# Kernel tuning notes

Hardware: AMD Instinct MI355X
Metric: run time of the kernel (lower is better)

The kernel has to match this reference:

```python
import jax, jax.numpy as jnp
import numpy as np

D = 1024      # embedding_dim
H = 16        # num_heads
DH = D // H   # head_dim
DFF = 4 * D
EPS = 1e-5


def setup_inputs() -> dict:
    key = jax.random.key(0)
    ks = jax.random.split(key, 10)
    B, T = 2, 2048
    s = 0.02
    return {
        "x": jax.random.normal(ks[0], (B, T, D), dtype=jnp.float32),
        "Wq": jax.random.normal(ks[1], (H, D, DH), dtype=jnp.float32) * s,
        "Wk": jax.random.normal(ks[2], (H, D, DH), dtype=jnp.float32) * s,
        "Wv": jax.random.normal(ks[3], (H, D, DH), dtype=jnp.float32) * s,
        "W1": jax.random.normal(ks[4], (D, DFF), dtype=jnp.float32) * s,
        "b1": jnp.zeros((DFF,), dtype=jnp.float32),
        "W2": jax.random.normal(ks[5], (DFF, D), dtype=jnp.float32) * s,
        "b2": jnp.zeros((D,), dtype=jnp.float32),
        "gamma1": jnp.ones((D,), dtype=jnp.float32),
        "beta1": jnp.zeros((D,), dtype=jnp.float32),
        "gamma2": jnp.ones((D,), dtype=jnp.float32),
        "beta2": jnp.zeros((D,), dtype=jnp.float32),
    }


def _layernorm(x, gamma, beta):
    # torch.var default is unbiased (ddof=1) -- faithful to LayerNorm1d
    mean = jnp.mean(x, axis=-1, keepdims=True)
    var = jnp.var(x, axis=-1, keepdims=True, ddof=1)
    return gamma * (x - mean) * jax.lax.rsqrt(var + EPS) + beta


def _block(x, Wq, Wk, Wv, W1, b1, W2, b2, gamma1, beta1, gamma2, beta2):
    B, T, _ = x.shape
    h = _layernorm(x, gamma1, beta1)
    # per-head projections stacked: [B,H,T,DH]
    Q = jnp.einsum('btd,hde->bhte', h, Wq)
    K = jnp.einsum('btd,hde->bhte', h, Wk)
    V = jnp.einsum('btd,hde->bhte', h, Wv)
    # NOTE: original scales by 1/sqrt(embedding_dim), NOT head_dim
    scores = jnp.einsum('bhqe,bhke->bhqk', Q, K) / jnp.sqrt(jnp.float32(D))
    causal = jnp.tril(jnp.ones((T, T), dtype=bool))
    scores = jnp.where(causal, scores, -jnp.inf)
    attn = jax.nn.softmax(scores, axis=-1)
    out = jnp.einsum('bhqk,bhke->bhqe', attn, V)
    # torch.cat over heads along last dim == transpose+reshape
    out = out.transpose(0, 2, 1, 3).reshape(B, T, D)
    x = x + out
    h2 = _layernorm(x, gamma2, beta2)
    ff = jax.nn.relu(h2 @ W1 + b1) @ W2 + b2  # dropout is identity at inference
    return x + ff


def reference(x, Wq, Wk, Wv, W1, b1, W2, b2, gamma1, beta1, gamma2, beta2):
    return _block(x, Wq, Wk, Wv, W1, b1, W2, b2, gamma1, beta1, gamma2, beta2)
```

## Files before the change

kernel.cpp:

```cpp
#include <hip/hip_runtime.h>

typedef unsigned short u16;
typedef __bf16 bf16;
typedef __attribute__((ext_vector_type(8))) __bf16 bf16x8;
typedef __attribute__((ext_vector_type(4))) float f32x4;
typedef __attribute__((ext_vector_type(8))) unsigned short u16x8;
typedef unsigned long long u64;

__device__ __forceinline__ float bf2f(u16 h) {
  return __uint_as_float(((unsigned int)h) << 16);
}
__device__ __forceinline__ u16 f2bf(float f) {
  unsigned int u = __float_as_uint(f);
  return (u16)((u + 0x7fffu + ((u >> 16) & 1u)) >> 16);
}
__device__ __forceinline__ u16 ld_cv(const void* p, size_t i, int f32) {
  return f32 ? f2bf(((const float*)p)[i]) : ((const u16*)p)[i];
}
__device__ __forceinline__ float ld_f(const void* p, size_t i, int f32) {
  return f32 ? ((const float*)p)[i] : bf2f(((const u16*)p)[i]);
}
__device__ __forceinline__ void async16(const u16* g, u16* l) {
  __builtin_amdgcn_global_load_lds(
      (const __attribute__((address_space(1))) unsigned int*)g,
      (__attribute__((address_space(3))) unsigned int*)l, 16, 0, 0);
}
__device__ __forceinline__ float exp2_raw(float x) {
  float r;
  asm("v_exp_f32 %0, %1" : "=v"(r) : "v"(x));
  return r;
}
__device__ __forceinline__ unsigned cvt_pk_bf16(float a, float b) {
  unsigned r;
  asm("v_cvt_pk_bf16_f32 %0, %1, %2" : "=v"(r) : "v"(a), "v"(b));
  return r;
}

__global__ void prep_kernel(const u16* __restrict__ x,
                            const void* __restrict__ Wq, const void* __restrict__ Wk,
                            const void* __restrict__ Wv, const void* __restrict__ W1,
                            const void* __restrict__ W2,
                            u16* __restrict__ WTq, u16* __restrict__ W1T,
                            u16* __restrict__ W2T,
                            const void* __restrict__ gamma1,
                            const void* __restrict__ beta1,
                            u16* __restrict__ hOut, int* __restrict__ flag) {
  __shared__ u16 tile[64][65];
  __shared__ int sm[4];
  __shared__ float ss[4], ssq[4];
  const int tid = threadIdx.x;
  int me = 0;
#pragma unroll
  for (int j = 0; j < 4; j++) {
    const u16 v = x[(tid * 4 + j) * 2];
    const int e = (v >> 7) & 0xFF;
    me = me > e ? me : e;
  }
#pragma unroll
  for (int off = 32; off > 0; off >>= 1) {
    const int o = __shfl_down(me, off);
    me = me > o ? me : o;
  }
  if ((tid & 63) == 0) sm[tid >> 6] = me;
  __syncthreads();
  const int a01 = sm[0] > sm[1] ? sm[0] : sm[1];
  const int a23 = sm[2] > sm[3] ? sm[2] : sm[3];
  const int f = ((a01 > a23 ? a01 : a23) >= 140) ? 1 : 0;
  if (blockIdx.x == 0 && tid == 0) *flag = f;

  const int bid = blockIdx.x;
  if (bid >= 2816) {
    const size_t row = bid - 2816;
    float v0, v1, v2, v3;
    if (f) {
      const float4 v = *((const float4*)x + row * 256 + tid);
      v0 = v.x; v1 = v.y; v2 = v.z; v3 = v.w;
    } else {
      const ushort4 u = *((const ushort4*)x + row * 256 + tid);
      v0 = bf2f(u.x); v1 = bf2f(u.y); v2 = bf2f(u.z); v3 = bf2f(u.w);
    }
    float s = v0 + v1 + v2 + v3;
    float sq = v0 * v0 + v1 * v1 + v2 * v2 + v3 * v3;
#pragma unroll
    for (int off = 32; off > 0; off >>= 1) {
      s += __shfl_down(s, off);
      sq += __shfl_down(sq, off);
    }
    if ((tid & 63) == 0) { ss[tid >> 6] = s; ssq[tid >> 6] = sq; }
    __syncthreads();
    s = ss[0] + ss[1] + ss[2] + ss[3];
    sq = ssq[0] + ssq[1] + ssq[2] + ssq[3];
    const float mean = s * (1.f / 1024.f);
    const float var = (sq - 1024.f * mean * mean) * (1.f / 1023.f);
    const float rs = rsqrtf(var + 1e-5f);
    const int c0 = tid * 4;
    ushort4 o;
    o.x = f2bf(ld_f(gamma1, c0 + 0, f) * (v0 - mean) * rs + ld_f(beta1, c0 + 0, f));
    o.y = f2bf(ld_f(gamma1, c0 + 1, f) * (v1 - mean) * rs + ld_f(beta1, c0 + 1, f));
    o.z = f2bf(ld_f(gamma1, c0 + 2, f) * (v2 - mean) * rs + ld_f(beta1, c0 + 2, f));
    o.w = f2bf(ld_f(gamma1, c0 + 3, f) * (v3 - mean) * rs + ld_f(beta1, c0 + 3, f));
    *(ushort4*)&hOut[row * 1024 + tid * 4] = o;
    return;
  }

  const void* src;
  u16* dst;
  int R, C, tcc, trr, rowbase;
  size_t sb = 0;
  if (bid < 768) {
    const int bx = bid & 15, wh = bid >> 4;
    const int w = wh >> 4, hh = wh & 15;
    trr = bx * 64;
    src = (w == 0) ? Wq : ((w == 1) ? Wk : Wv);
    sb = (size_t)hh * 65536;
    dst = WTq; R = 1024; C = 64; tcc = 0;
    rowbase = w * 1024 + hh * 64;
  } else if (bid < 1792) {
    const int j = bid - 768;
    src = W1; dst = W1T; R = 1024; C = 4096;
    tcc = (j & 63) * 64; trr = (j >> 6) * 64;
    rowbase = tcc;
  } else {
    const int j = bid - 1792;
    src = W2; dst = W2T; R = 4096; C = 1024;
    tcc = (j & 15) * 64; trr = (j >> 4) * 64;
    rowbase = tcc;
  }
  const int rr = tid >> 4, c4 = (tid & 15) * 4;
#pragma unroll
  for (int p = 0; p < 4; p++) {
    const int r = p * 16 + rr;
    const size_t off = sb + (size_t)(trr + r) * C + tcc + c4;
    if (f) {
      const float4 v = *(const float4*)((const float*)src + off);
      tile[r][c4 + 0] = f2bf(v.x);
      tile[r][c4 + 1] = f2bf(v.y);
      tile[r][c4 + 2] = f2bf(v.z);
      tile[r][c4 + 3] = f2bf(v.w);
    } else {
      const ushort4 u = *(const ushort4*)((const u16*)src + off);
      tile[r][c4 + 0] = u.x;
      tile[r][c4 + 1] = u.y;
      tile[r][c4 + 2] = u.z;
      tile[r][c4 + 3] = u.w;
    }
  }
  __syncthreads();
#pragma unroll
  for (int p = 0; p < 4; p++) {
    const int wrow = p * 16 + rr;
    ushort4 o;
    o.x = tile[c4 + 0][wrow];
    o.y = tile[c4 + 1][wrow];
    o.z = tile[c4 + 2][wrow];
    o.w = tile[c4 + 3][wrow];
    *(ushort4*)&dst[(size_t)(rowbase + wrow) * R + trr + c4] = o;
  }
}

template <int EPI, int WR, int WC, bool MS>
__launch_bounds__(WR * WC * 64)
__global__ void gemm_bt(const u16* __restrict__ A, const u16* __restrict__ B,
                        int K, int KLD, int NX, int N,
                        const void* __restrict__ bias, const u16* __restrict__ res,
                        void* __restrict__ out,
                        u16* __restrict__ Qo, u16* __restrict__ Ko, u16* __restrict__ Vto,
                        const int* __restrict__ flag) {
  constexpr int BM = WR * 64, BN = WC * 64, T = WR * WC * 64;
  constexpr int RPA = T / 4;
  constexpr int RAH = BM / RPA;
  constexpr int RBH = BN / RPA;
  __shared__ __align__(16) u16 As[BM * 64];
  __shared__ __align__(16) u16 Bs[BN * 64];
  const int tid = threadIdx.x;
  const int bid = blockIdx.x;
  const int sxp = NX >> 3;
  const int xcd = bid & 7, j9 = bid >> 3;
  int m0, n0, koff = 0, khb = 0;
  if (EPI == 3) {
    m0 = (xcd * 4 + (j9 & 3)) * BM;
    n0 = ((j9 >> 2) & 7) * BN;
    khb = (j9 >> 5) & 1;
    koff = khb * K;
  } else if (MS) {
    m0 = (xcd * sxp + j9 % sxp) * BM;
    n0 = (j9 / sxp) * BN;
  } else {
    n0 = (xcd * sxp + j9 % sxp) * BN;
    m0 = (j9 / sxp) * BM;
  }
  const int wave = tid >> 6, lane = tid & 63;
  const int wm = (wave / WC) * 64, wn = (wave % WC) * 64;
  const int lm = lane & 15, lq = lane >> 4;
  const int fb = (EPI == 1 || EPI == 2) ? *flag : 0;

  const f32x4 zero = {0.f, 0.f, 0.f, 0.f};
  f32x4 acc[4][4];
#pragma unroll
  for (int i = 0; i < 4; i++)
#pragma unroll
    for (int j = 0; j < 4; j++) acc[i][j] = zero;

  const int ar = tid >> 2;
  const int ac = ((tid & 3) ^ ((tid >> 3) & 3)) * 8;
  const u16* Ag = A + (size_t)(m0 + ar) * KLD + koff + ac;
  const u16* Bg = B + (size_t)(n0 + ar) * KLD + koff + ac;
  u16* AsP = &As[tid * 8];
  u16* BsP = &Bs[tid * 8];
  const int rq = (lq ^ ((lm >> 1) & 3)) * 8;

  for (int k0 = 0; k0 < K; k0 += 64) {
#pragma unroll
    for (int hh = 0; hh < 2; hh++) {
#pragma unroll
      for (int c = 0; c < RAH; c++)
        async16(Ag + k0 + hh * 32 + (size_t)c * RPA * KLD,
                AsP + hh * BM * 32 + c * RPA * 32);
#pragma unroll
      for (int c = 0; c < RBH; c++)
        async16(Bg + k0 + hh * 32 + (size_t)c * RPA * KLD,
                BsP + hh * BN * 32 + c * RPA * 32);
    }
    __syncthreads();
    bf16x8 a0[4], a1[4], b0[4], b1[4];
#pragma unroll
    for (int i = 0; i < 4; i++) {
      a0[i] = *(const bf16x8*)&As[(wm + i * 16 + lm) * 32 + rq];
      a1[i] = *(const bf16x8*)&As[BM * 32 + (wm + i * 16 + lm) * 32 + rq];
    }
#pragma unroll
    for (int i = 0; i < 4; i++) {
      b0[i] = *(const bf16x8*)&Bs[(wn + i * 16 + lm) * 32 + rq];
      b1[i] = *(const bf16x8*)&Bs[BN * 32 + (wn + i * 16 + lm) * 32 + rq];
    }
#pragma unroll
    for (int i = 0; i < 4; i++)
#pragma unroll
      for (int j = 0; j < 4; j++) {
        acc[i][j] = __builtin_amdgcn_mfma_f32_16x16x32_bf16(a0[i], b0[j], acc[i][j], 0, 0, 0);
        acc[i][j] = __builtin_amdgcn_mfma_f32_16x16x32_bf16(a1[i], b1[j], acc[i][j], 0, 0, 0);
      }
    __syncthreads();
  }

  if (EPI == 0) {
#pragma unroll
    for (int i = 0; i < 4; i++) {
      const int row0 = m0 + wm + i * 16 + lq * 4;
      const int bb = row0 >> 11, t0 = row0 & 2047;
#pragma unroll
      for (int j = 0; j < 4; j++) {
        const int col = n0 + wn + j * 16 + lm;
        const int w = col >> 10, nn = col & 1023;
        const int hh = nn >> 6, e = nn & 63;
        if (w == 2) {
          ushort4 v4;
          v4.x = f2bf(acc[i][j][0]);
          v4.y = f2bf(acc[i][j][1]);
          v4.z = f2bf(acc[i][j][2]);
          v4.w = f2bf(acc[i][j][3]);
          *(ushort4*)&Vto[(((size_t)(bb * 16 + hh)) * 64 + e) * 2048 + t0] = v4;
        } else {
          u16* dst = (w == 0) ? Qo : Ko;
          const float qs = (w == 0) ? 0.04508422f : 1.0f;
#pragma unroll
          for (int r = 0; r < 4; r++)
            dst[(((size_t)(bb * 16 + hh)) * 2048 + t0 + r) * 64 + e] =
                f2bf(acc[i][j][r] * qs);
        }
      }
    }
  } else if (EPI == 3) {
    u16* P = khb ? Ko : Qo;
#pragma unroll
    for (int i = 0; i < 4; i++) {
#pragma unroll
      for (int r = 0; r < 4; r++) {
        const int row = m0 + wm + i * 16 + lq * 4 + r;
#pragma unroll
        for (int j = 0; j < 4; j++) {
          const int col = n0 + wn + j * 16 + lm;
          P[(size_t)row * N + col] = f2bf(acc[i][j][r]);
        }
      }
    }
  } else {
#pragma unroll
    for (int i = 0; i < 4; i++) {
#pragma unroll
      for (int r = 0; r < 4; r++) {
        const int row = m0 + wm + i * 16 + lq * 4 + r;
#pragma unroll
        for (int j = 0; j < 4; j++) {
          const int col = n0 + wn + j * 16 + lm;
          const float c = acc[i][j][r];
          if (EPI == 1) {
            const float v = c + ld_f(bias, col, fb);
            ((u16*)out)[(size_t)row * N + col] = f2bf(v > 0.f ? v : 0.f);
          } else {
            const float v = c + ld_f(bias, col, fb) + bf2f(res[(size_t)row * N + col]);
            if (fb)
              ((float*)out)[(size_t)row * N + col] = v;
            else
              ((u16*)out)[(size_t)row * N + col] = f2bf(v);
          }
        }
      }
    }
  }
}

__launch_bounds__(256)
__global__ void ffn2_reduce(const u16* __restrict__ P0, const u16* __restrict__ P1,
                            const void* __restrict__ bias, const u16* __restrict__ res,
                            void* __restrict__ out, const int* __restrict__ flag) {
  const int f = *flag;
  const size_t i0 = ((size_t)blockIdx.x * 256 + threadIdx.x) * 8;
  const int col = (int)(i0 & 1023);
  const u16x8 a8 = *(const u16x8*)(P0 + i0);
  const u16x8 b8 = *(const u16x8*)(P1 + i0);
  const u16x8 r8 = *(const u16x8*)(res + i0);
  float v[8];
#pragma unroll
  for (int k = 0; k < 8; k++)
    v[k] = bf2f(a8[k]) + bf2f(b8[k]) + ld_f(bias, col + k, f) + bf2f(r8[k]);
  if (f) {
    float4 o0 = {v[0], v[1], v[2], v[3]};
    float4 o1 = {v[4], v[5], v[6], v[7]};
    *(float4*)((float*)out + i0) = o0;
    *(float4*)((float*)out + i0 + 4) = o1;
  } else {
    u16x8 o8;
#pragma unroll
    for (int k = 0; k < 8; k++) o8[k] = f2bf(v[k]);
    *(u16x8*)((u16*)out + i0) = o8;
  }
}

__launch_bounds__(256)
__global__ void attn_mfma(const u16* __restrict__ Q, const u16* __restrict__ K,
                          const u16* __restrict__ Vt, const void* __restrict__ xres,
                          const int* __restrict__ flag, u16* __restrict__ x2) {
  __shared__ __align__(16) unsigned char smem[35328];
  const int tid = threadIdx.x;
  const int wave = tid >> 6, lane = tid & 63;
  const int lm = lane & 15, quad = lane >> 4;
  const int bid = blockIdx.x;
  const int xcd = bid & 7, jj = bid >> 3;
  const int bh = xcd + 8 * (jj & 3);
  const int pair = jj >> 2;
  const int b = bh >> 4, h = bh & 15;
  const int f32in = *flag;

  u16* stw = (u16*)smem + wave * 4096;
  u16* Ksw = stw;
  u16* Vsw = stw + 2048;
  float (*Olds)[32][68] = (float(*)[32][68])smem;
  float (*Llds)[2][16] = (float(*)[2][16])(smem + 34816);

  const u16* Kbh = K + (size_t)bh * 131072;
  const u16* Vbh = Vt + (size_t)bh * 131072;
  const f32x4 zero = {0.f, 0.f, 0.f, 0.f};
  const int srow = lane >> 2;
  const int sch2 = (((lane & 3) ^ ((srow >> 1) & 3))) * 8;
  const int rk = (lm >> 1) & 3;

  union V8 { bf16x8 v; struct { u64 lo, hi; } q; };
  u16x8 ob;
#pragma unroll
  for (int k = 0; k < 8; k++) ob[k] = 0x3F80;
  const bf16x8 ones = *(const bf16x8*)&ob;

  auto stageK = [&](int t) {
    const int ks = t * 32;
#pragma unroll
    for (int hh2 = 0; hh2 < 2; hh2++)
#pragma unroll
      for (int c = 0; c < 2; c++)
        async16(Kbh + (size_t)(ks + c * 16 + srow) * 64 + hh2 * 32 + sch2,
                Ksw + hh2 * 1024 + c * 512 + lane * 8);
  };
  auto stageV = [&](int t) {
    const int ks = t * 32;
#pragma unroll
    for (int c = 0; c < 4; c++)
      async16(Vbh + (size_t)(c * 16 + srow) * 2048 + ks + sch2,
              Vsw + c * 512 + lane * 8);
  };

#pragma unroll 1
  for (int phase = 0; phase < 2; phase++) {
    const int qb = phase ? (63 - pair) : pair;
    const int qw0 = qb * 32;

    bf16x8 qf[2][2];
#pragma unroll
    for (int s = 0; s < 2; s++) {
      const u16* Qp = Q + ((size_t)bh * 2048 + qw0 + s * 16 + lm) * 64 + quad * 8;
      qf[s][0] = *(const bf16x8*)Qp;
      qf[s][1] = *(const bf16x8*)(Qp + 32);
    }
    __builtin_amdgcn_s_waitcnt(0x0F70);
    f32x4 ot[2][4];
    f32x4 al[2];
#pragma unroll
    for (int s = 0; s < 2; s++) {
#pragma unroll
      for (int j = 0; j < 4; j++) ot[s][j] = zero;
      al[s] = zero;
    }

    const int nt = qb + 1;
    const int si = (nt * wave) >> 2;
    const int ei = (nt * (wave + 1)) >> 2;

    if (si < ei) { stageK(si); stageV(si); }

#pragma unroll 1
    for (int t = si; t < ei; t++) {
      asm volatile("s_waitcnt vmcnt(4)" ::: "memory");
      bf16x8 kk[2][2];
#pragma unroll
      for (int hh = 0; hh < 2; hh++) {
        kk[hh][0] = *(const bf16x8*)&Ksw[(hh * 16 + lm) * 32 + (quad ^ rk) * 8];
        kk[hh][1] = *(const bf16x8*)&Ksw[1024 + (hh * 16 + lm) * 32 + (quad ^ rk) * 8];
      }
      f32x4 S[2][2];
#pragma unroll
      for (int s = 0; s < 2; s++)
#pragma unroll
        for (int hh = 0; hh < 2; hh++) {
          f32x4 a = zero;
          a = __builtin_amdgcn_mfma_f32_16x16x32_bf16(kk[hh][0], qf[s][0], a, 0, 0, 0);
          a = __builtin_amdgcn_mfma_f32_16x16x32_bf16(kk[hh][1], qf[s][1], a, 0, 0, 0);
          S[s][hh] = a;
        }
      __builtin_amdgcn_sched_barrier(0);
      const bool more = (t + 1 < ei);
      if (more) {
        stageK(t + 1);
        asm volatile("s_waitcnt vmcnt(4)" ::: "memory");
      } else {
        asm volatile("s_waitcnt vmcnt(0)" ::: "memory");
      }
      V8 vf[4];
#pragma unroll
      for (int j = 0; j < 4; j++) {
        vf[j].q.lo = *(const u64*)&Vsw[(j * 16 + lm) * 32 +
                                       (((quad >> 1)) ^ rk) * 8 + (quad & 1) * 4];
        vf[j].q.hi = *(const u64*)&Vsw[(j * 16 + lm) * 32 +
                                       (((quad >> 1) | 2) ^ rk) * 8 + (quad & 1) * 4];
      }
      const bool maskT = (t == qb);
#pragma unroll
      for (int s = 0; s < 2; s++) {
        float p[2][4];
#pragma unroll
        for (int hh = 0; hh < 2; hh++)
#pragma unroll
          for (int r = 0; r < 4; r++)
            p[hh][r] = exp2_raw(S[s][hh][r]);
        if (maskT) {
#pragma unroll
          for (int hh = 0; hh < 2; hh++)
#pragma unroll
            for (int r = 0; r < 4; r++)
              if (hh * 16 + quad * 4 + r > s * 16 + lm) p[hh][r] = 0.f;
        }
        unsigned pk[4];
        pk[0] = cvt_pk_bf16(p[0][0], p[0][1]);
        pk[1] = cvt_pk_bf16(p[0][2], p[0][3]);
        pk[2] = cvt_pk_bf16(p[1][0], p[1][1]);
        pk[3] = cvt_pk_bf16(p[1][2], p[1][3]);
        const bf16x8 pf = *(const bf16x8*)pk;
        al[s] = __builtin_amdgcn_mfma_f32_16x16x32_bf16(ones, pf, al[s], 0, 0, 0);
#pragma unroll
        for (int j = 0; j < 4; j++)
          ot[s][j] = __builtin_amdgcn_mfma_f32_16x16x32_bf16(vf[j].v, pf, ot[s][j], 0, 0, 0);
      }
      __builtin_amdgcn_sched_barrier(0);
      if (more) stageV(t + 1);
    }

    __syncthreads();

#pragma unroll
    for (int s = 0; s < 2; s++)
#pragma unroll
      for (int j = 0; j < 4; j++)
        *(f32x4*)&Olds[wave][s * 16 + lm][j * 16 + quad * 4] = ot[s][j];
    if (quad == 0) {
      Llds[wave][0][lm] = al[0][0];
      Llds[wave][1][lm] = al[1][0];
    }
    __syncthreads();
    const int q = tid >> 3;
    const int e0 = (tid & 7) * 8;
    f32x4 oa = zero, obv = zero;
#pragma unroll
    for (int w = 0; w < 4; w++) {
      oa += *(const f32x4*)&Olds[w][q][e0];
      obv += *(const f32x4*)&Olds[w][q][e0 + 4];
    }
    const float lt = Llds[0][q >> 4][q & 15] + Llds[1][q >> 4][q & 15] +
                     Llds[2][q >> 4][q & 15] + Llds[3][q >> 4][q & 15];
    const float linv = 1.f / lt;
    const size_t rowbase = ((size_t)(b * 2048 + qw0 + q)) * 1024 + h * 64 + e0;
    float xv[8];
    if (f32in) {
      const float* xf = (const float*)xres + rowbase;
      const float4 u0 = *(const float4*)xf;
      const float4 u1 = *(const float4*)(xf + 4);
      xv[0] = u0.x; xv[1] = u0.y; xv[2] = u0.z; xv[3] = u0.w;
      xv[4] = u1.x; xv[5] = u1.y; xv[6] = u1.z; xv[7] = u1.w;
    } else {
      const u16x8 u = *(const u16x8*)((const u16*)xres + rowbase);
#pragma unroll
      for (int k = 0; k < 8; k++) xv[k] = bf2f(u[k]);
    }
    u16x8 o8;
#pragma unroll
    for (int k = 0; k < 4; k++) o8[k] = f2bf(xv[k] + oa[k] * linv);
#pragma unroll
    for (int k = 0; k < 4; k++) o8[4 + k] = f2bf(xv[4 + k] + obv[k] * linv);
    *(u16x8*)&x2[rowbase] = o8;
    __syncthreads();
  }
}

__launch_bounds__(256)
__global__ void ln_kernel(const void* __restrict__ x, const void* __restrict__ gamma,
                          const void* __restrict__ beta, u16* __restrict__ out,
                          const int* __restrict__ flag, int xraw) {
  const size_t row = blockIdx.x;
  const int tid = threadIdx.x;
  const int f = *flag;
  const int fx = xraw ? f : 0;
  float v0, v1, v2, v3;
  if (fx) {
    const float4 v = *((const float4*)x + row * 256 + tid);
    v0 = v.x; v1 = v.y; v2 = v.z; v3 = v.w;
  } else {
    const ushort4 u = *((const ushort4*)x + row * 256 + tid);
    v0 = bf2f(u.x); v1 = bf2f(u.y); v2 = bf2f(u.z); v3 = bf2f(u.w);
  }
  float s = v0 + v1 + v2 + v3;
  float sq = v0 * v0 + v1 * v1 + v2 * v2 + v3 * v3;
#pragma unroll
  for (int off = 32; off > 0; off >>= 1) {
    s += __shfl_down(s, off);
    sq += __shfl_down(sq, off);
  }
  __shared__ float ss[4], ssq[4];
  if ((tid & 63) == 0) { ss[tid >> 6] = s; ssq[tid >> 6] = sq; }
  __syncthreads();
  s = ss[0] + ss[1] + ss[2] + ss[3];
  sq = ssq[0] + ssq[1] + ssq[2] + ssq[3];
  const float mean = s * (1.f / 1024.f);
  const float var = (sq - 1024.f * mean * mean) * (1.f / 1023.f);
  const float rs = rsqrtf(var + 1e-5f);
  const int c0 = tid * 4;
  ushort4 o;
  o.x = f2bf(ld_f(gamma, c0 + 0, f) * (v0 - mean) * rs + ld_f(beta, c0 + 0, f));
  o.y = f2bf(ld_f(gamma, c0 + 1, f) * (v1 - mean) * rs + ld_f(beta, c0 + 1, f));
  o.z = f2bf(ld_f(gamma, c0 + 2, f) * (v2 - mean) * rs + ld_f(beta, c0 + 2, f));
  o.w = f2bf(ld_f(gamma, c0 + 3, f) * (v3 - mean) * rs + ld_f(beta, c0 + 3, f));
  *(ushort4*)&out[row * 1024 + tid * 4] = o;
}

extern "C" void kernel_launch(void* const* d_in, const int* in_sizes, int n_in,
                              void* d_out, int out_size, void* d_ws, size_t ws_size,
                              hipStream_t stream) {
  const void* x      = d_in[0];
  const void* Wq     = d_in[1];
  const void* Wk     = d_in[2];
  const void* Wv     = d_in[3];
  const void* W1     = d_in[4];
  const void* b1     = d_in[5];
  const void* W2     = d_in[6];
  const void* b2     = d_in[7];
  const void* gamma1 = d_in[8];
  const void* beta1  = d_in[9];
  const void* gamma2 = d_in[10];
  const void* beta2  = d_in[11];
  u16* ws = (u16*)d_ws;

  const size_t M4 = 4194304;
  u16* h   = ws;
  u16* Qb  = ws + 1 * M4;
  u16* Kb  = ws + 2 * M4;
  u16* Vtb = ws + 3 * M4;
  u16* WTq = ws + 4 * M4;
  u16* x2  = ws + 4 * M4;
  u16* h2  = ws + 5 * M4;
  u16* W1T = ws + 6 * M4;
  u16* W2T = ws + 7 * M4;
  u16* ff1 = ws;
  u16* P0  = ws + 5 * M4;
  u16* P1  = ws + 6 * M4;
  int* flag = (int*)(ws + 8 * M4 + 9216);

  prep_kernel<<<6912, 256, 0, stream>>>((const u16*)x, Wq, Wk, Wv, W1, W2,
                                        WTq, W1T, W2T, gamma1, beta1, h, flag);
  gemm_bt<0, 2, 2, false><<<768, 256, 0, stream>>>(h, WTq, 1024, 1024, 24, 3072,
                                                   nullptr, nullptr, nullptr,
                                                   Qb, Kb, Vtb, flag);
  attn_mfma<<<1024, 256, 0, stream>>>(Qb, Kb, Vtb, x, flag, x2);
  ln_kernel<<<4096, 256, 0, stream>>>(x2, gamma2, beta2, h2, flag, 0);
  gemm_bt<1, 4, 2, false><<<512, 512, 0, stream>>>(h2, W1T, 1024, 1024, 32, 4096,
                                                   b1, nullptr, ff1,
                                                   nullptr, nullptr, nullptr, flag);
  gemm_bt<3, 2, 2, false><<<512, 256, 0, stream>>>(ff1, W2T, 2048, 4096, 8, 1024,
                                                   nullptr, nullptr, nullptr,
                                                   P0, P1, nullptr, flag);
  ffn2_reduce<<<2048, 256, 0, stream>>>(P0, P1, b2, x2, d_out, flag);
}
```

Before: 311.9 us.

## Split FFN2 K-halves across two wave groups with LDS reduction

Replaces the split-K FFN2 GEMM path (EPI==3, 256-thread blocks, K=2048 per block) with a dedicated 512-thread kernel. Two groups of four waves each take 1024 of the block's 2048-long K slice in separate LDS buffers. The groups' accumulators are then summed through shared memory before the bf16 partials are written. The aim is more waves in flight per tile and half the serial K loop per wave. The cost is more LDS per block (about 65KB), which may cap occupancy, plus an extra LDS reduction step.

After: 311.5 us. No clear change (-0.1%).

```diff
diff --git a/kernel.cpp b/kernel.cpp
--- a/kernel.cpp
+++ b/kernel.cpp
@@ -176,13 +176,8 @@
   const int bid = blockIdx.x;
   const int sxp = NX >> 3;
   const int xcd = bid & 7, j9 = bid >> 3;
-  int m0, n0, koff = 0, khb = 0;
-  if (EPI == 3) {
-    m0 = (xcd * 4 + (j9 & 3)) * BM;
-    n0 = ((j9 >> 2) & 7) * BN;
-    khb = (j9 >> 5) & 1;
-    koff = khb * K;
-  } else if (MS) {
+  int m0, n0;
+  if (MS) {
     m0 = (xcd * sxp + j9 % sxp) * BM;
     n0 = (j9 / sxp) * BN;
   } else {
@@ -203,8 +198,8 @@
 
   const int ar = tid >> 2;
   const int ac = ((tid & 3) ^ ((tid >> 3) & 3)) * 8;
-  const u16* Ag = A + (size_t)(m0 + ar) * KLD + koff + ac;
-  const u16* Bg = B + (size_t)(n0 + ar) * KLD + koff + ac;
+  const u16* Ag = A + (size_t)(m0 + ar) * KLD + ac;
+  const u16* Bg = B + (size_t)(n0 + ar) * KLD + ac;
   u16* AsP = &As[tid * 8];
   u16* BsP = &Bs[tid * 8];
   const int rq = (lq ^ ((lm >> 1) & 3)) * 8;
@@ -270,20 +265,6 @@
         }
       }
     }
-  } else if (EPI == 3) {
-    u16* P = khb ? Ko : Qo;
-#pragma unroll
-    for (int i = 0; i < 4; i++) {
-#pragma unroll
-      for (int r = 0; r < 4; r++) {
-        const int row = m0 + wm + i * 16 + lq * 4 + r;
-#pragma unroll
-        for (int j = 0; j < 4; j++) {
-          const int col = n0 + wn + j * 16 + lm;
-          P[(size_t)row * N + col] = f2bf(acc[i][j][r]);
-        }
-      }
-    }
   } else {
 #pragma unroll
     for (int i = 0; i < 4; i++) {
@@ -304,6 +285,102 @@
             else
               ((u16*)out)[(size_t)row * N + col] = f2bf(v);
           }
+        }
+      }
+    }
+  }
+}
+
+__launch_bounds__(512)
+__global__ void gemm_sk2(const u16* __restrict__ A, const u16* __restrict__ B,
+                         u16* __restrict__ P0, u16* __restrict__ P1) {
+  __shared__ __align__(16) unsigned char smem[66560];
+  const int tid = threadIdx.x;
+  const int bid = blockIdx.x;
+  const int xcd = bid & 7, j9 = bid >> 3;
+  const int m0 = (xcd * 4 + (j9 & 3)) * 128;
+  const int n0 = ((j9 >> 2) & 7) * 128;
+  const int khb = (j9 >> 5) & 1;
+  const int wave = tid >> 6, lane = tid & 63;
+  const int g = wave >> 2, lw = wave & 3;
+  const int gtid = tid & 255;
+  const int wm = (lw >> 1) * 64, wn = (lw & 1) * 64;
+  const int lm = lane & 15, lq = lane >> 4;
+
+  const f32x4 zero = {0.f, 0.f, 0.f, 0.f};
+  f32x4 acc[4][4];
+#pragma unroll
+  for (int i = 0; i < 4; i++)
+#pragma unroll
+    for (int j = 0; j < 4; j++) acc[i][j] = zero;
+
+  const int ar = gtid >> 2;
+  const int ac = ((gtid & 3) ^ ((gtid >> 3) & 3)) * 8;
+  const int koff = khb * 2048 + g * 1024;
+  const u16* Ag = A + (size_t)(m0 + ar) * 4096 + koff + ac;
+  const u16* Bg = B + (size_t)(n0 + ar) * 4096 + koff + ac;
+  u16* Sg = (u16*)smem + g * 16384;
+  u16* AsP = &Sg[gtid * 8];
+  u16* BsP = &Sg[8192 + gtid * 8];
+  const int rq = (lq ^ ((lm >> 1) & 3)) * 8;
+
+  for (int k0 = 0; k0 < 1024; k0 += 64) {
+#pragma unroll
+    for (int hh = 0; hh < 2; hh++) {
+#pragma unroll
+      for (int c = 0; c < 2; c++) {
+        async16(Ag + k0 + hh * 32 + (size_t)c * 64 * 4096,
+                AsP + hh * 4096 + c * 2048);
+        async16(Bg + k0 + hh * 32 + (size_t)c * 64 * 4096,
+                BsP + hh * 4096 + c * 2048);
+      }
+    }
+    __syncthreads();
+    bf16x8 a0[4], a1[4], b0[4], b1[4];
+#pragma unroll
+    for (int i = 0; i < 4; i++) {
+      a0[i] = *(const bf16x8*)&Sg[(wm + i * 16 + lm) * 32 + rq];
+      a1[i] = *(const bf16x8*)&Sg[4096 + (wm + i * 16 + lm) * 32 + rq];
+    }
+#pragma unroll
+    for (int i = 0; i < 4; i++) {
+      b0[i] = *(const bf16x8*)&Sg[8192 + (wn + i * 16 + lm) * 32 + rq];
+      b1[i] = *(const bf16x8*)&Sg[8192 + 4096 + (wn + i * 16 + lm) * 32 + rq];
+    }
+#pragma unroll
+    for (int i = 0; i < 4; i++)
+#pragma unroll
+      for (int j = 0; j < 4; j++) {
+        acc[i][j] = __builtin_amdgcn_mfma_f32_16x16x32_bf16(a0[i], b0[j], acc[i][j], 0, 0, 0);
+        acc[i][j] = __builtin_amdgcn_mfma_f32_16x16x32_bf16(a1[i], b1[j], acc[i][j], 0, 0, 0);
+      }
+    __syncthreads();
+  }
+
+  float* Ml = (float*)smem;
+  if (g == 1) {
+#pragma unroll
+    for (int i = 0; i < 4; i++)
+#pragma unroll
+      for (int j = 0; j < 4; j++)
+#pragma unroll
+        for (int r = 0; r < 4; r++)
+          Ml[(wm + i * 16 + lq * 4 + r) * 130 + wn + j * 16 + lm] = acc[i][j][r];
+  }
+  __syncthreads();
+  if (g == 0) {
+    u16* P = khb ? P1 : P0;
+#pragma unroll
+    for (int i = 0; i < 4; i++) {
+#pragma unroll
+      for (int r = 0; r < 4; r++) {
+        const int row = m0 + wm + i * 16 + lq * 4 + r;
+#pragma unroll
+        for (int j = 0; j < 4; j++) {
+          const int col = n0 + wn + j * 16 + lm;
+          const float v = acc[i][j][r] +
+                          Ml[(wm + i * 16 + lq * 4 + r) * 130 + wn + j * 16 + lm];
+          P[(size_t)row * 1024 + col] = f2bf(v);
         }
       }
     }
@@ -610,8 +687,6 @@
   gemm_bt<1, 4, 2, false><<<512, 512, 0, stream>>>(h2, W1T, 1024, 1024, 32, 4096,
                                                    b1, nullptr, ff1,
                                                    nullptr, nullptr, nullptr, flag);
-  gemm_bt<3, 2, 2, false><<<512, 256, 0, stream>>>(ff1, W2T, 2048, 4096, 8, 1024,
-                                                   nullptr, nullptr, nullptr,
-                                                   P0, P1, nullptr, flag);
+  gemm_sk2<<<512, 512, 0, stream>>>(ff1, W2T, P0, P1);
   ffn2_reduce<<<2048, 256, 0, stream>>>(P0, P1, b2, x2, d_out, flag);
 }
```
